# Kernel optimization log

Measured on AMD Instinct MI355X. Metric: run time of the kernel, lower is better.

## Reference

```python
import jax, jax.numpy as jnp
import numpy as np
from math import factorial

N_ATOM = 32768
NODE_DIM = 128
HID = 64
MUL = 16          # hidden multiplicity per irrep
INS = [(0,0,0),(0,2,2),(1,1,0),(1,1,1),(1,1,2),(2,0,2),(2,2,0),(2,2,1),(2,2,2)]  # (l1,l2,l_out)
W_NUMEL = len(INS)*MUL*MUL  # 2304 per-sample tp weights

# ---------- real Clebsch-Gordan coefficients (e3nn-style, Frobenius-normalized) ----------
def _su2_cg(j1,j2,j3,m1,m2,m3):
    if m3 != m1+m2 or not (abs(j1-j2) <= j3 <= j1+j2):
        return 0.0
    f = factorial
    pref = np.sqrt((2*j3+1)*f(j3+j1-j2)*f(j3-j1+j2)*f(j1+j2-j3)/f(j1+j2+j3+1))
    pref *= np.sqrt(f(j3+m3)*f(j3-m3)*f(j1-m1)*f(j1+m1)*f(j2-m2)*f(j2+m2))
    s = 0.0
    for v in range(max(0, j2-j3-m1, j1-j3+m2), min(j1+j2-j3, j1-m1, j2+m2)+1):
        s += (-1)**v/(f(v)*f(j1+j2-j3-v)*f(j1-m1-v)*f(j2+m2-v)*f(j3-j2+m1+v)*f(j3-j1-m2+v))
    return pref*s

def _r2c(l):
    q = np.zeros((2*l+1,2*l+1), dtype=complex)
    for m in range(-l, 0):
        q[l+m, l+abs(m)] = 1/np.sqrt(2); q[l+m, l-abs(m)] = -1j/np.sqrt(2)
    q[l, l] = 1.0
    for m in range(1, l+1):
        q[l+m, l+abs(m)] = (-1)**m/np.sqrt(2); q[l+m, l-abs(m)] = 1j*(-1)**m/np.sqrt(2)
    return (-1j)**l * q

def real_cg(l1, l2, l3):
    C = np.zeros((2*l1+1,2*l2+1,2*l3+1), dtype=complex)
    for m1 in range(-l1, l1+1):
        for m2 in range(-l2, l2+1):
            m3 = m1+m2
            if abs(m3) <= l3:
                C[l1+m1, l2+m2, l3+m3] = _su2_cg(l1,l2,l3,m1,m2,m3)
    Cr = np.einsum('ij,kl,nm,ikn->jlm', _r2c(l1), _r2c(l2), np.conj(_r2c(l3)), C)
    re, im = np.real(Cr), np.imag(Cr)
    out = re if np.linalg.norm(re) >= np.linalg.norm(im) else im
    return (out / np.linalg.norm(out)).astype(np.float32)

_CG = {ins: real_cg(*ins) for ins in set(INS)}
# change of basis: irreps 1x0e+1x1e+1x2e (dim 9) -> cartesian 3x3 rank-2 tensor
_QF = np.concatenate([np.sqrt(2*l+1)*real_cg(l,1,1) for l in range(3)], 0).reshape(9,9).astype(np.float32)
_PERM = np.array([2,0,1])  # e3nn (y,z,x) -> cartesian (x,y,z)


def setup_inputs() -> dict:
    key = jax.random.key(0)
    ks = jax.random.split(key, 12)
    n = lambda k, s: jax.random.normal(k, s, dtype=jnp.float32)
    return {
        "x_scalar": n(ks[0], (N_ATOM, NODE_DIM)),
        "x_spherical": n(ks[1], (N_ATOM, 128 + 64*3 + 32*5)),
        "w_pre0": n(ks[2], (128, MUL)),
        "w_pre1": n(ks[3], (64, MUL)),
        "w_pre2": n(ks[4], (32, MUL)),
        "gw1": n(ks[5], (NODE_DIM, HID)) / float(np.sqrt(NODE_DIM)),
        "gb1": jnp.zeros((HID,), jnp.float32),
        "gw2": n(ks[6], (HID, W_NUMEL)) / float(np.sqrt(HID)),
        "gb2": jnp.zeros((W_NUMEL,), jnp.float32),
        "wpost0": n(ks[7], (3*MUL, 1)),
        "wpost1": n(ks[8], (2*MUL, 1)),
        "wpost2": n(ks[9], (4*MUL, 1)),
    }


def reference(x_scalar, x_spherical, w_pre0, w_pre1, w_pre2, gw1, gb1, gw2, gb2, wpost0, wpost1, wpost2):
    N = x_scalar.shape[0]
    # split edge irreps 128x0e + 64x1o + 32x2e
    x0 = x_spherical[:, :128]
    x1 = x_spherical[:, 128:320].reshape(N, 64, 3)
    x2 = x_spherical[:, 320:].reshape(N, 32, 5)
    # pre o3.Linear (per-l channel mixing, fan-in normalized)
    h = [
        (x0 @ w_pre0)[:, :, None] / float(np.sqrt(128.0)),              # [N,16,1] 0e
        jnp.einsum('num,uv->nvm', x1, w_pre1) / float(np.sqrt(64.0)),    # [N,16,3] 1o
        jnp.einsum('num,uv->nvm', x2, w_pre2) / float(np.sqrt(32.0)),    # [N,16,5] 2e
    ]
    # gate MLP -> per-sample tp weights [N, n_ins, u, w]
    g = (jax.nn.silu(x_scalar @ gw1 + gb1) @ gw2 + gb2).reshape(N, len(INS), MUL, MUL)
    # 'uuw' CG tensor product
    outs = {0: [], 1: [], 2: []}
    inv_sqrt_mul = float(1.0 / np.sqrt(MUL))
    for idx, (i, j, lo) in enumerate(INS):
        C = jnp.asarray(_CG[(i, j, lo)])
        o = jnp.einsum('nuw,abm,nua,nub->nwm', g[:, idx], C, h[i], h[j]) * inv_sqrt_mul
        outs[lo].append(o)
    # post o3.Linear: (48x0e + 32x1e + 64x2e) -> 1x0e + 1x1e + 1x2e
    wpost = [wpost0, wpost1, wpost2]
    ys = []
    for lo in range(3):
        z = jnp.concatenate(outs[lo], axis=1)                       # [N, n_paths*MUL, 2lo+1]
        y = jnp.einsum('num,uv->nvm', z, wpost[lo]) / float(np.sqrt(z.shape[1]))
        ys.append(y.reshape(N, 2*lo+1))
    atom_out = jnp.concatenate(ys, axis=1)                           # [N,9]
    # change of basis to cartesian rank-2 tensor + axis reindexing
    res = (atom_out @ jnp.asarray(_QF)).reshape(N, 3, 3)
    return res[:, _PERM][:, :, _PERM]
```

## Files before the change

### kernel.cpp

```cpp
#include <hip/hip_runtime.h>

#define NA 32768

typedef float  f32x4  __attribute__((ext_vector_type(4)));
typedef __bf16 bf16x8 __attribute__((ext_vector_type(8)));
typedef unsigned short u16x8 __attribute__((ext_vector_type(8)));
typedef unsigned short u16x4 __attribute__((ext_vector_type(4)));


__device__ __forceinline__ unsigned short bf16u(float f) {
    unsigned int x = __float_as_uint(f);
    x += 0x7FFFu + ((x >> 16) & 1u);
    return (unsigned short)(x >> 16);
}
__device__ __forceinline__ unsigned short cvt1(float f) {
    return __builtin_bit_cast(unsigned short, (__bf16)f);
}
__device__ __forceinline__ f32x4 MFMA16(u16x8 a, u16x8 b, f32x4 c) {
    return __builtin_amdgcn_mfma_f32_16x16x32_bf16(
        __builtin_bit_cast(bf16x8, a), __builtin_bit_cast(bf16x8, b), c, 0, 0, 0);
}

__global__ void setup_kernel(const float* __restrict__ gw1,
                             const float* __restrict__ gw2, const float* __restrict__ gb2,
                             const float* __restrict__ w_pre0, const float* __restrict__ w_pre1,
                             const float* __restrict__ w_pre2,
                             const float* __restrict__ wpost0, const float* __restrict__ wpost1,
                             const float* __restrict__ wpost2,
                             unsigned short* __restrict__ wsS, float* __restrict__ b2p)
{
    const int t = blockIdx.x * 256 + threadIdx.x;
    const int LO[9]  = {0,2,0,1,2,2,0,1,2};
    const int POS[9] = {0,0,1,0,1,2,2,1,3};
    const float SCALE[3] = {0.036084391824351615f,
                            0.04419417382415922f,
                            0.03125f};
    if (t < 8192) {
        const int j = t & 7, lane = (t >> 3) & 63, kt = (t >> 9) & 3, ct = t >> 11;
        const int k = kt * 32 + ((lane >> 4) & 3) * 8 + j;
        const int n = ct * 16 + (lane & 15);
        wsS[t] = bf16u(gw1[k * 64 + n]);
    } else if (t < 17408) {
        const int q = t - 8192;
        const int j = q & 7, lane = (q >> 3) & 63, kt = (q >> 9) & 1, ct = q >> 10;
        const int k = kt * 32 + ((lane >> 4) & 3) * 8 + j;
        const int idx = ct, u = lane & 15;
        const int lo = LO[idx];
        const float* wp = (lo == 0) ? wpost0 : (lo == 1) ? wpost1 : wpost2;
        const float* wv = wp + POS[idx] * 16;
        const float* gsrc = gw2 + (size_t)k * 2304 + idx * 256 + u * 16;
        float s = 0.f;
        for (int w = 0; w < 16; ++w) s = fmaf(gsrc[w], wv[w], s);
        wsS[8192 + q] = bf16u(s * SCALE[lo]);
    } else if (t < 19456) {
        const int q = t - 17408;
        const int j = q & 7, lane = (q >> 3) & 63, kt = q >> 9;
        const int k = kt * 32 + ((lane >> 4) & 3) * 8 + j;
        wsS[17408 + q] = bf16u(w_pre0[k * 16 + (lane & 15)] * 0.08838834764831845f);
    } else if (t < 20480) {
        const int q = t - 19456;
        const int j = q & 7, lane = (q >> 3) & 63, kt = q >> 9;
        const int k = kt * 32 + ((lane >> 4) & 3) * 8 + j;
        wsS[19456 + q] = bf16u(w_pre1[k * 16 + (lane & 15)] * 0.125f);
    } else if (t < 20992) {
        const int q = t - 20480;
        const int j = q & 7, lane = (q >> 3) & 63;
        const int k = ((lane >> 4) & 3) * 8 + j;
        wsS[20480 + q] = bf16u(w_pre2[k * 16 + (lane & 15)] * 0.17677669529663687f);
    } else if (t < 21136) {
        const int e = t - 20992;
        const int idx = e >> 4, u = e & 15;
        const int lo = LO[idx];
        const float* wp = (lo == 0) ? wpost0 : (lo == 1) ? wpost1 : wpost2;
        const float* wv = wp + POS[idx] * 16;
        const float* bsrc = gb2 + idx * 256 + u * 16;
        float sb = 0.f;
        for (int w = 0; w < 16; ++w) sb = fmaf(bsrc[w], wv[w], sb);
        b2p[e] = sb * SCALE[lo];
    }
}

#define ROWQ 488
#define ROWS 136
#define SHOFF 7808

__global__ __launch_bounds__(256) void csc_kernel(
    const float* __restrict__ x_scalar, const float* __restrict__ x_sph,
    const float* __restrict__ gb1,
    const unsigned short* __restrict__ wsS, const float* __restrict__ b2p,
    float* __restrict__ out)
{
    __shared__ __align__(16) unsigned short buf[4][8960];

    const int lane = threadIdx.x & 63;
    const int wvi  = threadIdx.x >> 6;
    const int lm = lane & 15, lg = lane >> 4;
    const int n0 = (blockIdx.x * 4 + wvi) * 16;
    unsigned short* __restrict__ B = buf[wvi];

    {
        const float* __restrict__ src = x_sph + (size_t)n0 * 480;
#pragma unroll
        for (int i = 0; i < 30; ++i) {
            const int idx4 = i * 64 + lane;
            const int row = idx4 / 120, col4 = idx4 - row * 120;
            const float4 v = *(const float4*)(src + (size_t)idx4 * 4);
            const u16x4 w = { cvt1(v.x), cvt1(v.y), cvt1(v.z), cvt1(v.w) };
            *(u16x4*)&B[row * ROWQ + col4 * 4] = w;
        }
    }

    u16x8 f0[4];
#pragma unroll
    for (int kt = 0; kt < 4; ++kt)
        f0[kt] = *(const u16x8*)&B[lm * ROWQ + kt * 32 + lg * 8];
    u16x8 f1[3][2];
#pragma unroll
    for (int kt = 0; kt < 2; ++kt) {
        const int base = lm * ROWQ + 128 + 96 * kt + 24 * lg;
        const u16x8 sA = *(const u16x8*)&B[base];
        const u16x8 sB = *(const u16x8*)&B[base + 8];
        const u16x8 sC = *(const u16x8*)&B[base + 16];
        unsigned short span[24];
#pragma unroll
        for (int e = 0; e < 8; ++e) { span[e] = sA[e]; span[8 + e] = sB[e]; span[16 + e] = sC[e]; }
#pragma unroll
        for (int m = 0; m < 3; ++m) {
            u16x8 f;
#pragma unroll
            for (int j = 0; j < 8; ++j) f[j] = span[3 * j + m];
            f1[m][kt] = f;
        }
    }
    u16x8 f2[5];
    {
        const int base = lm * ROWQ + 320 + 40 * lg;
        unsigned short span[40];
#pragma unroll
        for (int c = 0; c < 5; ++c) {
            const u16x8 s = *(const u16x8*)&B[base + c * 8];
#pragma unroll
            for (int e = 0; e < 8; ++e) span[c * 8 + e] = s[e];
        }
#pragma unroll
        for (int m = 0; m < 5; ++m) {
            u16x8 f;
#pragma unroll
            for (int j = 0; j < 8; ++j) f[j] = span[5 * j + m];
            f2[m] = f;
        }
    }

    f32x4 acc0 = (f32x4){0.f,0.f,0.f,0.f};
#pragma unroll
    for (int kt = 0; kt < 4; ++kt)
        acc0 = MFMA16(f0[kt], *(const u16x8*)(wsS + 17408 + (size_t)(kt*64+lane)*8), acc0);
    f32x4 accP[3];
#pragma unroll
    for (int m = 0; m < 3; ++m) {
        f32x4 acc = (f32x4){0.f,0.f,0.f,0.f};
#pragma unroll
        for (int kt = 0; kt < 2; ++kt)
            acc = MFMA16(f1[m][kt], *(const u16x8*)(wsS + 19456 + (size_t)(kt*64+lane)*8), acc);
        accP[m] = acc;
    }
    f32x4 accQ[5];
#pragma unroll
    for (int m = 0; m < 5; ++m)
        accQ[m] = MFMA16(f2[m], *(const u16x8*)(wsS + 20480 + (size_t)lane*8),
                         (f32x4){0.f,0.f,0.f,0.f});

    {
        const float* __restrict__ src = x_scalar + (size_t)n0 * 128;
#pragma unroll
        for (int i = 0; i < 8; ++i) {
            const int idx4 = i * 64 + lane;
            const int row = idx4 >> 5, col4 = idx4 & 31;
            const float4 v = *(const float4*)(src + (size_t)idx4 * 4);
            const u16x4 w = { cvt1(v.x), cvt1(v.y), cvt1(v.z), cvt1(v.w) };
            *(u16x4*)&B[row * ROWS + col4 * 4] = w;
        }
    }

    f32x4 accA0, accA1, accA2, accA3;
    {
        const float b0 = gb1[lm], b1 = gb1[16 + lm], bv2 = gb1[32 + lm], b3 = gb1[48 + lm];
        accA0 = (f32x4){b0,b0,b0,b0}; accA1 = (f32x4){b1,b1,b1,b1};
        accA2 = (f32x4){bv2,bv2,bv2,bv2}; accA3 = (f32x4){b3,b3,b3,b3};
    }
#pragma unroll
    for (int kt = 0; kt < 4; ++kt) {
        const u16x8 af = *(const u16x8*)&B[lm * ROWS + kt * 32 + lg * 8];
        accA0 = MFMA16(af, *(const u16x8*)(wsS + (size_t)((0*4+kt)*64+lane)*8), accA0);
        accA1 = MFMA16(af, *(const u16x8*)(wsS + (size_t)((1*4+kt)*64+lane)*8), accA1);
        accA2 = MFMA16(af, *(const u16x8*)(wsS + (size_t)((2*4+kt)*64+lane)*8), accA2);
        accA3 = MFMA16(af, *(const u16x8*)(wsS + (size_t)((3*4+kt)*64+lane)*8), accA3);
    }
#pragma unroll
    for (int r = 0; r < 4; ++r) {
        const int atom = lg * 4 + r;
        const float v0 = accA0[r], v1 = accA1[r], v2 = accA2[r], v3 = accA3[r];
        B[SHOFF + atom * 72 +  0 + lm] = cvt1(v0 / (1.f + __expf(-v0)));
        B[SHOFF + atom * 72 + 16 + lm] = cvt1(v1 / (1.f + __expf(-v1)));
        B[SHOFF + atom * 72 + 32 + lm] = cvt1(v2 / (1.f + __expf(-v2)));
        B[SHOFF + atom * 72 + 48 + lm] = cvt1(v3 / (1.f + __expf(-v3)));
    }

    const u16x8 hf0 = *(const u16x8*)&B[SHOFF + lm * 72 + lg * 8];
    const u16x8 hf1 = *(const u16x8*)&B[SHOFF + lm * 72 + 32 + lg * 8];
    f32x4 gB0, gB1, gB2, gB4, gB5, gB6, gB8;
#define INITB(ACC, CT) { const float b = b2p[(CT)*16 + lm]; ACC = (f32x4){b,b,b,b}; }
    INITB(gB0,0) INITB(gB1,1) INITB(gB2,2) INITB(gB4,4) INITB(gB5,5) INITB(gB6,6) INITB(gB8,8)
#define DOB(ACC, CT) \
    ACC = MFMA16(hf0, *(const u16x8*)(wsS + 8192 + (size_t)(((CT)*2+0)*64+lane)*8), ACC); \
    ACC = MFMA16(hf1, *(const u16x8*)(wsS + 8192 + (size_t)(((CT)*2+1)*64+lane)*8), ACC);
    DOB(gB0,0) DOB(gB1,1) DOB(gB2,2) DOB(gB4,4) DOB(gB5,5) DOB(gB6,6) DOB(gB8,8)

    const float C110 = 0.5773502691896258f;
    const float C220 = 0.4472135954999579f;
    const float Ca = 0.31622776601683794f, Cb = 0.18257418583505536f;
    const float A2 = 0.2390457218668787f, B2c = 0.20701966780270626f, D2 = 0.11952286093343936f;
    const float is3 = 0.5773502691896258f, is6 = 0.4082482904638631f, is2 = 0.7071067811865476f;

#pragma unroll
    for (int r = 0; r < 4; ++r) {
        const int row = lg * 4 + r;
        const float h0 = acc0[r];
        const float p0 = accP[0][r], p1 = accP[1][r], p2 = accP[2][r];
        const float q0 = accQ[0][r], q1 = accQ[1][r], q2 = accQ[2][r],
                    q3 = accQ[3][r], q4 = accQ[4][r];
        const float G0 = gB0[r], G1 = gB1[r], G2 = gB2[r], G4 = gB4[r],
                    G5 = gB5[r], G6 = gB6[r], G8 = gB8[r];

        float y0 = G0 * h0 * h0
                 + G2 * C110 * (p0*p0 + p1*p1 + p2*p2)
                 + G6 * C220 * (q0*q0 + q1*q1 + q2*q2 + q3*q3 + q4*q4);
        float z0, z1, z2, z3, z4;
        {
            const float c15 = C220 * h0 * (G1 + G5);
            z0 = c15 * q0; z1 = c15 * q1; z2 = c15 * q2; z3 = c15 * q3; z4 = c15 * q4;
        }
        z0 = fmaf(G4, 2.f*Ca*p0*p2, z0);
        z1 = fmaf(G4, 2.f*Ca*p0*p1, z1);
        z2 = fmaf(G4, Cb*(2.f*p1*p1 - p0*p0 - p2*p2), z2);
        z3 = fmaf(G4, 2.f*Ca*p2*p1, z3);
        z4 = fmaf(G4, Ca*(p2*p2 - p0*p0), z4);
        z0 = fmaf(G8, -2.f*A2*q0*q2 + 2.f*B2c*q1*q3, z0);
        z1 = fmaf(G8,  2.f*B2c*(q0*q3 - q4*q1) + 2.f*D2*q1*q2, z1);
        z2 = fmaf(G8,  A2*(q2*q2 - q0*q0 - q4*q4) + D2*(q1*q1 + q3*q3), z2);
        z3 = fmaf(G8,  2.f*B2c*(q0*q1 + q3*q4) + 2.f*D2*q2*q3, z3);
        z4 = fmaf(G8, -2.f*A2*q2*q4 + B2c*(q3*q3 - q1*q1), z4);

#pragma unroll
        for (int msk = 1; msk <= 8; msk <<= 1) {
            y0 += __shfl_xor(y0, msk, 64);
            z0 += __shfl_xor(z0, msk, 64);
            z1 += __shfl_xor(z1, msk, 64);
            z2 += __shfl_xor(z2, msk, 64);
            z3 += __shfl_xor(z3, msk, 64);
            z4 += __shfl_xor(z4, msk, 64);
        }

        const float c0 = y0*is3 - z2*is6 - z4*is2;
        const float c4 = y0*is3 + 2.f*z2*is6;
        const float c8 = y0*is3 - z2*is6 + z4*is2;
        const float c1 = z1*is2, c2v = z0*is2, c5 = z3*is2;
        if (lm < 9) {
            const float val = (lm==0)?c8 : (lm==1)?c2v : (lm==2)?c5 : (lm==3)?c2v
                            : (lm==4)?c0 : (lm==5)?c1 : (lm==6)?c5 : (lm==7)?c1 : c4;
            out[(size_t)(n0 + row) * 9 + lm] = val;
        }
    }
}

extern "C" void kernel_launch(void* const* d_in, const int* in_sizes, int n_in,
                              void* d_out, int out_size, void* d_ws, size_t ws_size,
                              hipStream_t stream) {
    const float* x_scalar = (const float*)d_in[0];
    const float* x_sph    = (const float*)d_in[1];
    const float* w_pre0   = (const float*)d_in[2];
    const float* w_pre1   = (const float*)d_in[3];
    const float* w_pre2   = (const float*)d_in[4];
    const float* gw1      = (const float*)d_in[5];
    const float* gb1      = (const float*)d_in[6];
    const float* gw2      = (const float*)d_in[7];
    const float* gb2      = (const float*)d_in[8];
    const float* wpost0   = (const float*)d_in[9];
    const float* wpost1   = (const float*)d_in[10];
    const float* wpost2   = (const float*)d_in[11];

    unsigned short* wsS = (unsigned short*)d_ws;
    float* b2p = (float*)((char*)d_ws + 41984);

    setup_kernel<<<83, 256, 0, stream>>>(gw1, gw2, gb2, w_pre0, w_pre1, w_pre2,
                                         wpost0, wpost1, wpost2, wsS, b2p);
    csc_kernel<<<NA / 64, 256, 0, stream>>>(x_scalar, x_sph, gb1, wsS, b2p, (float*)d_out);
}
```

Baseline: 27.56 us.

## Stage x_spherical per irrep block in smaller LDS buffer to raise occupancy

Splits the staging of x_spherical into three passes (l=0, l=1, l=2 segments). Each pass reuses one 200-element-per-row LDS region, and each segment's MFMAs run right after its fragments are extracted. This shrinks per-wave LDS from 8960 to 4352 shorts and adds a launch_bounds minimum of 4 blocks per SM, aiming for more resident waves to hide memory latency. Loads are batched into register arrays before conversion so more global loads are in flight at once. The risks are extra register pressure from the batched float4 arrays and more serialized load-then-compute phases within each wave.

New measurement: 27.14 us, median of 3. Within noise of the previous version (-1.5%).

```diff
diff --git a/kernel.cpp b/kernel.cpp
--- a/kernel.cpp
+++ b/kernel.cpp
@@ -80,17 +80,16 @@
     }
 }
 
-#define ROWQ 488
-#define ROWS 136
-#define SHOFF 7808
-
-__global__ __launch_bounds__(256) void csc_kernel(
+#define RR 200
+#define SHO 3200
+
+__global__ __launch_bounds__(256, 4) void csc_kernel(
     const float* __restrict__ x_scalar, const float* __restrict__ x_sph,
     const float* __restrict__ gb1,
     const unsigned short* __restrict__ wsS, const float* __restrict__ b2p,
     float* __restrict__ out)
 {
-    __shared__ __align__(16) unsigned short buf[4][8960];
+    __shared__ __align__(16) unsigned short buf[4][4352];
 
     const int lane = threadIdx.x & 63;
     const int wvi  = threadIdx.x >> 6;
@@ -98,44 +97,97 @@
     const int n0 = (blockIdx.x * 4 + wvi) * 16;
     unsigned short* __restrict__ B = buf[wvi];
 
-    {
-        const float* __restrict__ src = x_sph + (size_t)n0 * 480;
-#pragma unroll
-        for (int i = 0; i < 30; ++i) {
-            const int idx4 = i * 64 + lane;
-            const int row = idx4 / 120, col4 = idx4 - row * 120;
-            const float4 v = *(const float4*)(src + (size_t)idx4 * 4);
-            const u16x4 w = { cvt1(v.x), cvt1(v.y), cvt1(v.z), cvt1(v.w) };
-            *(u16x4*)&B[row * ROWQ + col4 * 4] = w;
-        }
-    }
-
-    u16x8 f0[4];
-#pragma unroll
-    for (int kt = 0; kt < 4; ++kt)
-        f0[kt] = *(const u16x8*)&B[lm * ROWQ + kt * 32 + lg * 8];
-    u16x8 f1[3][2];
-#pragma unroll
-    for (int kt = 0; kt < 2; ++kt) {
-        const int base = lm * ROWQ + 128 + 96 * kt + 24 * lg;
-        const u16x8 sA = *(const u16x8*)&B[base];
-        const u16x8 sB = *(const u16x8*)&B[base + 8];
-        const u16x8 sC = *(const u16x8*)&B[base + 16];
-        unsigned short span[24];
-#pragma unroll
-        for (int e = 0; e < 8; ++e) { span[e] = sA[e]; span[8 + e] = sB[e]; span[16 + e] = sC[e]; }
+    const float* __restrict__ srcq = x_sph + (size_t)n0 * 480;
+
+    {
+        float4 v[8];
+#pragma unroll
+        for (int i = 0; i < 8; ++i) {
+            const int idx4 = i * 64 + lane;
+            const int row = idx4 >> 5, col4 = idx4 & 31;
+            v[i] = *(const float4*)(srcq + (size_t)row * 480 + col4 * 4);
+        }
+#pragma unroll
+        for (int i = 0; i < 8; ++i) {
+            const int idx4 = i * 64 + lane;
+            const int row = idx4 >> 5, col4 = idx4 & 31;
+            const u16x4 w = { cvt1(v[i].x), cvt1(v[i].y), cvt1(v[i].z), cvt1(v[i].w) };
+            *(u16x4*)&B[row * RR + col4 * 4] = w;
+        }
+    }
+    f32x4 acc0 = (f32x4){0.f,0.f,0.f,0.f};
+#pragma unroll
+    for (int kt = 0; kt < 4; ++kt) {
+        const u16x8 f = *(const u16x8*)&B[lm * RR + kt * 32 + lg * 8];
+        acc0 = MFMA16(f, *(const u16x8*)(wsS + 17408 + (size_t)(kt*64+lane)*8), acc0);
+    }
+
+    {
+        float4 v[12];
+#pragma unroll
+        for (int i = 0; i < 12; ++i) {
+            const int idx4 = i * 64 + lane;
+            const int row = idx4 / 48, col4 = idx4 - row * 48;
+            v[i] = *(const float4*)(srcq + (size_t)row * 480 + 128 + col4 * 4);
+        }
+#pragma unroll
+        for (int i = 0; i < 12; ++i) {
+            const int idx4 = i * 64 + lane;
+            const int row = idx4 / 48, col4 = idx4 - row * 48;
+            const u16x4 w = { cvt1(v[i].x), cvt1(v[i].y), cvt1(v[i].z), cvt1(v[i].w) };
+            *(u16x4*)&B[row * RR + col4 * 4] = w;
+        }
+    }
+    f32x4 accP[3];
+    {
+        u16x8 f1[3][2];
+#pragma unroll
+        for (int kt = 0; kt < 2; ++kt) {
+            const int base = lm * RR + 96 * kt + 24 * lg;
+            const u16x8 sA = *(const u16x8*)&B[base];
+            const u16x8 sB = *(const u16x8*)&B[base + 8];
+            const u16x8 sC = *(const u16x8*)&B[base + 16];
+            unsigned short span[24];
+#pragma unroll
+            for (int e = 0; e < 8; ++e) { span[e] = sA[e]; span[8+e] = sB[e]; span[16+e] = sC[e]; }
+#pragma unroll
+            for (int m = 0; m < 3; ++m) {
+                u16x8 f;
+#pragma unroll
+                for (int j = 0; j < 8; ++j) f[j] = span[3 * j + m];
+                f1[m][kt] = f;
+            }
+        }
 #pragma unroll
         for (int m = 0; m < 3; ++m) {
-            u16x8 f;
-#pragma unroll
-            for (int j = 0; j < 8; ++j) f[j] = span[3 * j + m];
-            f1[m][kt] = f;
-        }
-    }
-    u16x8 f2[5];
-    {
-        const int base = lm * ROWQ + 320 + 40 * lg;
+            f32x4 acc = (f32x4){0.f,0.f,0.f,0.f};
+#pragma unroll
+            for (int kt = 0; kt < 2; ++kt)
+                acc = MFMA16(f1[m][kt], *(const u16x8*)(wsS + 19456 + (size_t)(kt*64+lane)*8), acc);
+            accP[m] = acc;
+        }
+    }
+
+    {
+        float4 v[10];
+#pragma unroll
+        for (int i = 0; i < 10; ++i) {
+            const int idx4 = i * 64 + lane;
+            const int row = idx4 / 40, col4 = idx4 - row * 40;
+            v[i] = *(const float4*)(srcq + (size_t)row * 480 + 320 + col4 * 4);
+        }
+#pragma unroll
+        for (int i = 0; i < 10; ++i) {
+            const int idx4 = i * 64 + lane;
+            const int row = idx4 / 40, col4 = idx4 - row * 40;
+            const u16x4 w = { cvt1(v[i].x), cvt1(v[i].y), cvt1(v[i].z), cvt1(v[i].w) };
+            *(u16x4*)&B[row * RR + col4 * 4] = w;
+        }
+    }
+    f32x4 accQ[5];
+    {
         unsigned short span[40];
+        const int base = lm * RR + 40 * lg;
 #pragma unroll
         for (int c = 0; c < 5; ++c) {
             const u16x8 s = *(const u16x8*)&B[base + c * 8];
@@ -147,38 +199,25 @@
             u16x8 f;
 #pragma unroll
             for (int j = 0; j < 8; ++j) f[j] = span[5 * j + m];
-            f2[m] = f;
-        }
-    }
-
-    f32x4 acc0 = (f32x4){0.f,0.f,0.f,0.f};
-#pragma unroll
-    for (int kt = 0; kt < 4; ++kt)
-        acc0 = MFMA16(f0[kt], *(const u16x8*)(wsS + 17408 + (size_t)(kt*64+lane)*8), acc0);
-    f32x4 accP[3];
-#pragma unroll
-    for (int m = 0; m < 3; ++m) {
-        f32x4 acc = (f32x4){0.f,0.f,0.f,0.f};
-#pragma unroll
-        for (int kt = 0; kt < 2; ++kt)
-            acc = MFMA16(f1[m][kt], *(const u16x8*)(wsS + 19456 + (size_t)(kt*64+lane)*8), acc);
-        accP[m] = acc;
-    }
-    f32x4 accQ[5];
-#pragma unroll
-    for (int m = 0; m < 5; ++m)
-        accQ[m] = MFMA16(f2[m], *(const u16x8*)(wsS + 20480 + (size_t)lane*8),
-                         (f32x4){0.f,0.f,0.f,0.f});
+            accQ[m] = MFMA16(f, *(const u16x8*)(wsS + 20480 + (size_t)lane*8),
+                             (f32x4){0.f,0.f,0.f,0.f});
+        }
+    }
 
     {
         const float* __restrict__ src = x_scalar + (size_t)n0 * 128;
+        float4 v[8];
 #pragma unroll
         for (int i = 0; i < 8; ++i) {
             const int idx4 = i * 64 + lane;
+            v[i] = *(const float4*)(src + (size_t)idx4 * 4);
+        }
+#pragma unroll
+        for (int i = 0; i < 8; ++i) {
+            const int idx4 = i * 64 + lane;
             const int row = idx4 >> 5, col4 = idx4 & 31;
-            const float4 v = *(const float4*)(src + (size_t)idx4 * 4);
-            const u16x4 w = { cvt1(v.x), cvt1(v.y), cvt1(v.z), cvt1(v.w) };
-            *(u16x4*)&B[row * ROWS + col4 * 4] = w;
+            const u16x4 w = { cvt1(v[i].x), cvt1(v[i].y), cvt1(v[i].z), cvt1(v[i].w) };
+            *(u16x4*)&B[row * RR + col4 * 4] = w;
         }
     }
 
@@ -190,7 +229,7 @@
     }
 #pragma unroll
     for (int kt = 0; kt < 4; ++kt) {
-        const u16x8 af = *(const u16x8*)&B[lm * ROWS + kt * 32 + lg * 8];
+        const u16x8 af = *(const u16x8*)&B[lm * RR + kt * 32 + lg * 8];
         accA0 = MFMA16(af, *(const u16x8*)(wsS + (size_t)((0*4+kt)*64+lane)*8), accA0);
         accA1 = MFMA16(af, *(const u16x8*)(wsS + (size_t)((1*4+kt)*64+lane)*8), accA1);
         accA2 = MFMA16(af, *(const u16x8*)(wsS + (size_t)((2*4+kt)*64+lane)*8), accA2);
@@ -200,14 +239,14 @@
     for (int r = 0; r < 4; ++r) {
         const int atom = lg * 4 + r;
         const float v0 = accA0[r], v1 = accA1[r], v2 = accA2[r], v3 = accA3[r];
-        B[SHOFF + atom * 72 +  0 + lm] = cvt1(v0 / (1.f + __expf(-v0)));
-        B[SHOFF + atom * 72 + 16 + lm] = cvt1(v1 / (1.f + __expf(-v1)));
-        B[SHOFF + atom * 72 + 32 + lm] = cvt1(v2 / (1.f + __expf(-v2)));
-        B[SHOFF + atom * 72 + 48 + lm] = cvt1(v3 / (1.f + __expf(-v3)));
-    }
-
-    const u16x8 hf0 = *(const u16x8*)&B[SHOFF + lm * 72 + lg * 8];
-    const u16x8 hf1 = *(const u16x8*)&B[SHOFF + lm * 72 + 32 + lg * 8];
+        B[SHO + atom * 72 +  0 + lm] = cvt1(v0 / (1.f + __expf(-v0)));
+        B[SHO + atom * 72 + 16 + lm] = cvt1(v1 / (1.f + __expf(-v1)));
+        B[SHO + atom * 72 + 32 + lm] = cvt1(v2 / (1.f + __expf(-v2)));
+        B[SHO + atom * 72 + 48 + lm] = cvt1(v3 / (1.f + __expf(-v3)));
+    }
+
+    const u16x8 hf0 = *(const u16x8*)&B[SHO + lm * 72 + lg * 8];
+    const u16x8 hf1 = *(const u16x8*)&B[SHO + lm * 72 + 32 + lg * 8];
     f32x4 gB0, gB1, gB2, gB4, gB5, gB6, gB8;
 #define INITB(ACC, CT) { const float b = b2p[(CT)*16 + lm]; ACC = (f32x4){b,b,b,b}; }
     INITB(gB0,0) INITB(gB1,1) INITB(gB2,2) INITB(gB4,4) INITB(gB5,5) INITB(gB6,6) INITB(gB8,8)
```
